# Optimization experiments

Hardware: AMD Instinct MI355X
Metric: run time of the kernel (lower is better)

The kernel has to match this reference:

```python
import jax, jax.numpy as jnp
import numpy as np

H, D, HID, DIN = 2, 32, 64, 128
NQ, NA, NK = 100000, 200000, 200000
E_KQ, E_QK, E_QA, E_AQ = 800000, 800000, 400000, 400000
EP, EN = 100000, 100000


def setup_inputs() -> dict:
    key = jax.random.key(0)
    ks = jax.random.split(key, 32)
    f = lambda i, shape, s=0.05: jax.random.normal(ks[i], shape, dtype=jnp.float32) * s
    ri = lambda i, n, hi: jax.random.randint(ks[i], (n,), 0, hi)
    return {
        'xq': f(0, (NQ, DIN), 1.0), 'xa': f(1, (NA, DIN), 1.0), 'xk': f(2, (NK, DIN), 1.0),
        'lin_w': f(3, (3, DIN, HID)), 'lin_b': f(4, (3, HID)),
        'k_w': f(5, (3, HID, HID)), 'k_b': f(6, (3, HID)),
        'q_w': f(7, (3, HID, HID)), 'q_b': f(8, (3, HID)),
        'v_w': f(9, (3, HID, HID)), 'v_b': f(10, (3, HID)),
        'a_w': f(11, (3, HID, HID)), 'a_b': f(12, (3, HID)),
        'a_rel': f(13, (4, H, D, D), 0.2), 'm_rel': f(14, (4, H, D, D), 0.2),
        'p_rel': jnp.ones((4, H), dtype=jnp.float32),  # PyG init: ones
        'skip': jnp.ones((3,), dtype=jnp.float32),     # PyG init: ones
        'ei_kq_src': ri(15, E_KQ, NK), 'ei_kq_dst': ri(16, E_KQ, NQ),
        'ei_qk_src': ri(17, E_QK, NQ), 'ei_qk_dst': ri(18, E_QK, NA * 0 + NK),
        'ei_qa_src': ri(19, E_QA, NQ), 'ei_qa_dst': ri(20, E_QA, NA),
        'ei_aq_src': ri(21, E_AQ, NA), 'ei_aq_dst': ri(22, E_AQ, NQ),
        'pos_src': ri(23, EP, NQ), 'pos_dst': ri(24, EP, NA),
        'neg_src': ri(25, EN, NQ), 'neg_dst': ri(26, EN, NA),
    }


def _seg_softmax(alpha, dst, n):
    # softmax over incoming edges per destination node (per head)
    m = jax.ops.segment_max(alpha, dst, num_segments=n)
    m = jnp.where(jnp.isfinite(m), m, 0.0)
    e = jnp.exp(alpha - m[dst])
    s = jax.ops.segment_sum(e, dst, num_segments=n)
    return e / (s[dst] + 1e-16)


def hgt_forward(xq, xa, xk, lin_w, lin_b, k_w, k_b, q_w, q_b, v_w, v_b, a_w, a_b,
                a_rel, m_rel, p_rel, skip, edges):
    # node types: 0=question, 1=answer, 2=knowledge
    xs = [jax.nn.relu(x @ lin_w[i] + lin_b[i]) for i, x in enumerate([xq, xa, xk])]
    ns = [x.shape[0] for x in xs]
    k = [(x @ k_w[i] + k_b[i]).reshape(-1, H, D) for i, x in enumerate(xs)]
    q = [(x @ q_w[i] + q_b[i]).reshape(-1, H, D) for i, x in enumerate(xs)]
    v = [(x @ v_w[i] + v_b[i]).reshape(-1, H, D) for i, x in enumerate(xs)]
    out = [jnp.zeros((n, H, D), dtype=xs[0].dtype) for n in ns]
    scale = 1.0 / jnp.sqrt(jnp.float32(D))
    for st, dt, r, es, ed in edges:
        # per-edge-type head-wise key/value transforms (applied at node level)
        k_rel = jnp.einsum('nhd,hde->nhe', k[st], a_rel[r])
        v_rel = jnp.einsum('nhd,hde->nhe', v[st], m_rel[r])
        alpha = (q[dt][ed] * k_rel[es]).sum(-1) * p_rel[r] * scale  # [E,H]
        a = _seg_softmax(alpha, ed, ns[dt])
        msg = a[:, :, None] * v_rel[es]  # [E,H,D]
        out[dt] = out[dt] + jax.ops.segment_sum(msg, ed, num_segments=ns[dt])
    z = []
    for i in range(3):
        o = jax.nn.gelu(out[i].reshape(-1, H * D), approximate=False) @ a_w[i] + a_b[i]
        beta = jax.nn.sigmoid(skip[i])
        z.append(beta * o + (1.0 - beta) * xs[i])
    return z  # [z_question, z_answer, z_knowledge]; note: HGT.forward never applies self.lin


def reference(xq, xa, xk, lin_w, lin_b, k_w, k_b, q_w, q_b, v_w, v_b, a_w, a_b,
              a_rel, m_rel, p_rel, skip,
              ei_kq_src, ei_kq_dst, ei_qk_src, ei_qk_dst, ei_qa_src, ei_qa_dst,
              ei_aq_src, ei_aq_dst, pos_src, pos_dst, neg_src, neg_dst):
    edges = [
        (2, 0, 0, ei_kq_src, ei_kq_dst),  # knowledge -> question
        (0, 2, 1, ei_qk_src, ei_qk_dst),  # question -> knowledge
        (0, 1, 2, ei_qa_src, ei_qa_dst),  # question -> answer
        (1, 0, 3, ei_aq_src, ei_aq_dst),  # answer -> question
    ]
    zq, za, zk = hgt_forward(xq, xa, xk, lin_w, lin_b, k_w, k_b, q_w, q_b, v_w, v_b,
                             a_w, a_b, a_rel, m_rel, p_rel, skip, edges)
    pos_pred = jax.nn.sigmoid((zq[pos_src] * za[pos_dst]).sum(-1))
    neg_pred = jax.nn.sigmoid((zq[neg_src] * za[neg_dst]).sum(-1))
    return (pos_pred, neg_pred, zq, za, zk)
```

## Files before the change

### kernel.cpp

```cpp
#include <hip/hip_runtime.h>
#include <math.h>

namespace {

constexpr int NQn = 100000, NAn = 200000, NKn = 200000;
constexpr int EPc = 100000, ENc = 100000;
constexpr int ETOT = 2400000, NSEG = 600000;
constexpr int LIN_THREADS = 7813 * 256;

constexpr long XSB_OFF  = 0;
constexpr long OUTB_OFF = 16000000;
constexpr long QBF_OFF  = 32000000;
constexpr long KV_OFF   = 48000000;
constexpr long ZB_OFF   = 86500000;
constexpr long WTB_OFF  = 96200000;
constexpr long WFB_OFF  = 96250000;
constexpr long INT_OFF  = 96300000;
constexpr long DEG_I  = 0;
constexpr long OFFS_I = 600064;
constexpr long PART_I = 1200128;
constexpr long RANK_I = 1201152;
constexpr long CSRC_I = 3601152;

constexpr int LINT_U = 0;
constexpr int QT_U   = 24576;
constexpr int AT_U   = 36864;
constexpr int WFT_U  = 49152;

__constant__ long c_rbase[4] = {0, 200000, 300032, 400064};

typedef __attribute__((ext_vector_type(8))) short bf16x8;
typedef __attribute__((ext_vector_type(4))) float f32x4;
typedef __attribute__((ext_vector_type(4))) unsigned int u32x4;
typedef __attribute__((ext_vector_type(2))) unsigned int u32x2;

__device__ inline f32x4 mfma16(bf16x8 a, bf16x8 b, f32x4 c) {
    return __builtin_amdgcn_mfma_f32_16x16x32_bf16(a, b, c, 0, 0, 0);
}

__device__ inline float gelu_f(float x) {
    return 0.5f * x * (1.0f + erff(x * 0.7071067811865475f));
}
__device__ inline float bf2f(unsigned short u) {
    return __uint_as_float(((unsigned)u) << 16);
}
__device__ inline unsigned short f2bf(float f) {
    unsigned u = __float_as_uint(f);
    return (unsigned short)((u + 0x7fffu + ((u >> 16) & 1u)) >> 16);
}

__device__ inline void type_of_block128(int b, int& t, int& n0) {
    if (b < 782)       { t = 0; n0 = b * 128; }
    else if (b < 2345) { t = 1; n0 = (b - 782) * 128; }
    else               { t = 2; n0 = (b - 2345) * 128; }
}
__device__ inline void type_of_block64(int b, int& t, int& n0) {
    if (b < 1563)      { t = 0; n0 = b * 64; }
    else if (b < 4688) { t = 1; n0 = (b - 1563) * 64; }
    else               { t = 2; n0 = (b - 4688) * 64; }
}

template<int K>
__device__ inline void stage_bf16(unsigned short* lds, const unsigned short* src,
                                  int n0, int n, int tid)
{
    constexpr int CPR = K / 8;
    for (int c = tid; c < 128 * CPR; c += 256) {
        int row = c / CPR, kc = c % CPR;
        int node = n0 + row; if (node > n - 1) node = n - 1;
        uint4 v = *(const uint4*)&src[(long)node * K + kc * 8];
        int byte = (row * K + kc * 8) * 2;
        *(uint4*)((char*)lds + (byte ^ ((row & 7) << 4))) = v;
    }
}

__device__ inline void stage_out_gelu(unsigned short* lds, const unsigned short* src,
                                      int n0, int n, int tid)
{
    for (int c = tid; c < 128 * 8; c += 256) {
        int row = c >> 3, kc = c & 7;
        int node = n0 + row; if (node > n - 1) node = n - 1;
        uint4 v = *(const uint4*)&src[(long)node * 64 + kc * 8];
        float f0 = gelu_f(bf2f((unsigned short)(v.x & 0xffffu)));
        float f1 = gelu_f(bf2f((unsigned short)(v.x >> 16)));
        float f2 = gelu_f(bf2f((unsigned short)(v.y & 0xffffu)));
        float f3 = gelu_f(bf2f((unsigned short)(v.y >> 16)));
        float f4 = gelu_f(bf2f((unsigned short)(v.z & 0xffffu)));
        float f5 = gelu_f(bf2f((unsigned short)(v.z >> 16)));
        float f6 = gelu_f(bf2f((unsigned short)(v.w & 0xffffu)));
        float f7 = gelu_f(bf2f((unsigned short)(v.w >> 16)));
        uint4 o;
        o.x = (unsigned)f2bf(f0) | ((unsigned)f2bf(f1) << 16);
        o.y = (unsigned)f2bf(f2) | ((unsigned)f2bf(f3) << 16);
        o.z = (unsigned)f2bf(f4) | ((unsigned)f2bf(f5) << 16);
        o.w = (unsigned)f2bf(f6) | ((unsigned)f2bf(f7) << 16);
        int byte = (row * 64 + kc * 8) * 2;
        *(uint4*)((char*)lds + (byte ^ ((row & 7) << 4))) = o;
    }
}

template<int K, int ROWS>
__device__ inline void stage_f32_nt(unsigned short* lds, const float* src,
                                    int n0, int n, int tid)
{
    constexpr int CPR = K / 8;
    for (int c = tid; c < ROWS * CPR; c += 256) {
        int row = c / CPR, kc = c % CPR;
        int node = n0 + row; if (node > n - 1) node = n - 1;
        const f32x4* sp = (const f32x4*)&src[(long)node * K + kc * 8];
        f32x4 f0 = __builtin_nontemporal_load(sp);
        f32x4 f1 = __builtin_nontemporal_load(sp + 1);
        uint4 v;
        v.x = (unsigned)f2bf(f0.x) | ((unsigned)f2bf(f0.y) << 16);
        v.y = (unsigned)f2bf(f0.z) | ((unsigned)f2bf(f0.w) << 16);
        v.z = (unsigned)f2bf(f1.x) | ((unsigned)f2bf(f1.y) << 16);
        v.w = (unsigned)f2bf(f1.z) | ((unsigned)f2bf(f1.w) << 16);
        int byte = (row * K + kc * 8) * 2;
        *(uint4*)((char*)lds + (byte ^ ((row & 7) << 4))) = v;
    }
}

template<int N, int K>
__device__ inline void stage_w(unsigned short* lds, const unsigned short* wt, int tid)
{
    constexpr int CPR = K / 8;
    for (int c = tid; c < N * CPR; c += 256) {
        int nr = c / CPR, kc = c % CPR;
        uint4 v = *(const uint4*)&wt[nr * K + kc * 8];
        int byte = (nr * K + kc * 8) * 2;
        *(uint4*)((char*)lds + (byte ^ ((nr & 7) << 4))) = v;
    }
}

template<int K, int NF, int MF>
__device__ inline void mfma_coreT(const unsigned short* ldsX, const unsigned short* ldsW,
                                  f32x4 (&acc)[MF][NF], int lane, int w)
{
    const int lrow = lane & 15, lk = (lane >> 4) * 8;
    #pragma unroll
    for (int ks = 0; ks < K / 32; ++ks) {
        bf16x8 a[MF], b[NF];
        #pragma unroll
        for (int mf = 0; mf < MF; ++mf) {
            int row = w * (16 * MF) + mf * 16 + lrow;
            int byte = (row * K + ks * 32 + lk) * 2;
            a[mf] = *(const bf16x8*)((const char*)ldsX + (byte ^ ((row & 7) << 4)));
        }
        #pragma unroll
        for (int nf = 0; nf < NF; ++nf) {
            int nr = nf * 16 + lrow;
            int byte = (nr * K + ks * 32 + lk) * 2;
            b[nf] = *(const bf16x8*)((const char*)ldsW + (byte ^ ((nr & 7) << 4)));
        }
        #pragma unroll
        for (int mf = 0; mf < MF; ++mf)
            #pragma unroll
            for (int nf = 0; nf < NF; ++nf)
                acc[mf][nf] = mfma16(b[nf], a[mf], acc[mf][nf]);
    }
}

__device__ inline void edge_map(int gid,
                                const int* __restrict__ s0, const int* __restrict__ d0,
                                const int* __restrict__ s1, const int* __restrict__ d1,
                                const int* __restrict__ s2, const int* __restrict__ d2,
                                const int* __restrict__ s3, const int* __restrict__ d3,
                                int& seg, int& s)
{
    if (gid < 800000)       { seg = d0[gid];                    s = s0[gid]; }
    else if (gid < 1600000) { seg = 100000 + d1[gid - 800000];  s = s1[gid - 800000]; }
    else if (gid < 2000000) { seg = 300000 + d2[gid - 1600000]; s = s2[gid - 1600000]; }
    else                    { seg = 500000 + d3[gid - 2000000]; s = s3[gid - 2000000]; }
}
__device__ inline int edge_seg(int gid,
                               const int* __restrict__ d0, const int* __restrict__ d1,
                               const int* __restrict__ d2, const int* __restrict__ d3)
{
    if (gid < 800000)       return d0[gid];
    else if (gid < 1600000) return 100000 + d1[gid - 800000];
    else if (gid < 2000000) return 300000 + d2[gid - 1600000];
    else                    return 500000 + d3[gid - 2000000];
}

__global__ void prep_count(const float* __restrict__ lin_w, const float* __restrict__ q_w,
                           const float* __restrict__ a_w,
                           const float* __restrict__ kw, const float* __restrict__ kb,
                           const float* __restrict__ vw, const float* __restrict__ vb,
                           const float* __restrict__ a_rel, const float* __restrict__ m_rel,
                           unsigned short* __restrict__ wtb, float* __restrict__ wfb,
                           const int* __restrict__ d0, const int* __restrict__ d1,
                           const int* __restrict__ d2, const int* __restrict__ d3,
                           int* __restrict__ deg, int* __restrict__ rank)
{
    const int tid = threadIdx.x;
    if (blockIdx.x < 4) {
        const int r = blockIdx.x;
        const int st_tab[4] = {2, 0, 0, 1};
        const int st = st_tab[r];
        for (int idx = tid; idx < 8192; idx += 256) {
            int d = idx >> 7, c = idx & 127;
            int i = c >> 1, which = c & 1;
            int h = i >> 5, e = i & 31;
            const float* w   = (which ? vw : kw) + st * 4096;
            const float* rel = (which ? m_rel : a_rel) + r * 2048;
            float s = 0.f;
            #pragma unroll
            for (int c32 = 0; c32 < 32; ++c32)
                s += w[d * 64 + h * 32 + c32] * rel[h * 1024 + c32 * 32 + e];
            wtb[WFT_U + r * 8192 + c * 64 + d] = f2bf(s);
        }
        for (int idx = tid; idx < 128; idx += 256) {
            int i = idx >> 1, which = idx & 1;
            int h = i >> 5, e = i & 31;
            const float* b   = (which ? vb : kb) + st * 64;
            const float* rel = (which ? m_rel : a_rel) + r * 2048;
            float s = 0.f;
            #pragma unroll
            for (int c32 = 0; c32 < 32; ++c32)
                s += b[h * 32 + c32] * rel[h * 1024 + c32 * 32 + e];
            wfb[r * 128 + idx] = s;
        }
    } else if (blockIdx.x < 196) {
        int i = (blockIdx.x - 4) * 256 + tid;
        if (i < 24576) {
            int t = i / 8192, rem = i % 8192, nn = rem >> 7, kk = rem & 127;
            wtb[LINT_U + i] = f2bf(lin_w[t * 8192 + kk * 64 + nn]);
        } else if (i < 36864) {
            int j = i - 24576;
            int t = j / 4096, rem = j % 4096, nn = rem >> 6, kk = rem & 63;
            wtb[QT_U + j] = f2bf(q_w[t * 4096 + kk * 64 + nn]);
        } else if (i < 49152) {
            int j = i - 36864;
            int t = j / 4096, rem = j % 4096, nn = rem >> 6, kk = rem & 63;
            wtb[AT_U + j] = f2bf(a_w[t * 4096 + kk * 64 + nn]);
        }
    } else {
        int gid = (blockIdx.x - 196) * 256 + tid;
        if (gid < ETOT) {
            int seg = edge_seg(gid, d0, d1, d2, d3);
            rank[gid] = atomicAdd(&deg[seg], 1);
        }
    }
}

__global__ void __launch_bounds__(256)
lin_fill(const int* __restrict__ s0, const int* __restrict__ d0,
         const int* __restrict__ s1, const int* __restrict__ d1,
         const int* __restrict__ s2, const int* __restrict__ d2,
         const int* __restrict__ s3, const int* __restrict__ d3,
         const int* __restrict__ off, const int* __restrict__ rank,
         int* __restrict__ csrc,
         const float* __restrict__ xq, const float* __restrict__ xa,
         const float* __restrict__ xk, const unsigned short* __restrict__ wtb,
         const float* __restrict__ lin_b, unsigned short* __restrict__ xsb)
{
    __shared__ unsigned short ldsX[64 * 128];
    __shared__ unsigned short ldsW[64 * 128];
    const int tid = threadIdx.x;
    const int gid = blockIdx.x * 256 + tid;

    int segA, sA;
    edge_map(gid, s0, d0, s1, d1, s2, d2, s3, d3, segA, sA);
    int rkA = rank[gid];
    int offA = off[segA];
    const int gidB = gid + LIN_THREADS;
    const bool hasB = gidB < ETOT;
    int segB = 0, sB = 0, rkB = 0, offB = 0;
    if (hasB) {
        edge_map(gidB, s0, d0, s1, d1, s2, d2, s3, d3, segB, sB);
        rkB = rank[gidB];
        offB = off[segB];
    }

    int t, n0; type_of_block64(blockIdx.x, t, n0);
    const int cnt[3] = {NQn, NAn, NKn};
    const long noff[3] = {0, NQn, NQn + NAn};
    const float* X = (t == 0) ? xq : (t == 1) ? xa : xk;
    const int n = cnt[t];

    stage_w<64, 128>(ldsW, wtb + LINT_U + t * 8192, tid);
    stage_f32_nt<128, 64>(ldsX, X, n0, n, tid);
    __syncthreads();

    csrc[offA + rkA] = sA;
    if (hasB) csrc[offB + rkB] = sB;

    const int w = tid >> 6, lane = tid & 63;
    f32x4 acc[1][4] = {};
    mfma_coreT<128, 4, 1>(ldsX, ldsW, acc, lane, w);

    const int nodeL = lane & 15, colG = (lane >> 4) * 4;
    int node = n0 + w * 16 + nodeL;
    if (node < n) {
        #pragma unroll
        for (int nf = 0; nf < 4; ++nf) {
            int col0 = nf * 16 + colG;
            float4 bv = *(const float4*)&lin_b[t * 64 + col0];
            ushort4 o;
            o.x = f2bf(fmaxf(acc[0][nf][0] + bv.x, 0.f));
            o.y = f2bf(fmaxf(acc[0][nf][1] + bv.y, 0.f));
            o.z = f2bf(fmaxf(acc[0][nf][2] + bv.z, 0.f));
            o.w = f2bf(fmaxf(acc[0][nf][3] + bv.w, 0.f));
            *(ushort4*)&xsb[(noff[t] + node) * 64 + col0] = o;
        }
    }
}

__global__ void __launch_bounds__(256)
qkv_split(const unsigned short* __restrict__ xsb, const unsigned short* __restrict__ wtb,
          const float* __restrict__ q_b, const float* __restrict__ wfb,
          unsigned short* __restrict__ qbf, unsigned short* __restrict__ kvb)
{
    __shared__ unsigned short ldsX[128 * 64];
    __shared__ unsigned short ldsW[128 * 64];
    const int cnt[3] = {NQn, NAn, NKn};
    const long noff[3] = {0, NQn, NQn + NAn};
    const int tid = threadIdx.x;
    const int w = tid >> 6, lane = tid & 63;
    const int nodeL = lane & 15, colG = (lane >> 4) * 4;
    const int b = blockIdx.x;

    if (b < 3908) {
        int t, n0; type_of_block128(b, t, n0);
        const int n = cnt[t];
        stage_bf16<64>(ldsX, xsb + noff[t] * 64, n0, n, tid);
        stage_w<64, 64>(ldsW, wtb + QT_U + t * 4096, tid);
        __syncthreads();

        f32x4 acc[2][4] = {};
        mfma_coreT<64, 4, 2>(ldsX, ldsW, acc, lane, w);
        #pragma unroll
        for (int mf = 0; mf < 2; ++mf) {
            int node = n0 + w * 32 + mf * 16 + nodeL;
            if (node < n) {
                #pragma unroll
                for (int nf = 0; nf < 4; ++nf) {
                    int col0 = nf * 16 + colG;
                    float4 bv = *(const float4*)&q_b[t * 64 + col0];
                    ushort4 o;
                    o.x = f2bf(acc[mf][nf][0] + bv.x);
                    o.y = f2bf(acc[mf][nf][1] + bv.y);
                    o.z = f2bf(acc[mf][nf][2] + bv.z);
                    o.w = f2bf(acc[mf][nf][3] + bv.w);
                    *(ushort4*)&qbf[(noff[t] + node) * 64 + col0] = o;
                }
            }
        }
    } else {
        int kb = b - 3908, r, lb;
        if (kb < 1563)      { r = 0; lb = kb; }
        else if (kb < 2345) { r = 1; lb = kb - 1563; }
        else if (kb < 3127) { r = 2; lb = kb - 2345; }
        else                { r = 3; lb = kb - 3127; }
        const int stt[4] = {2, 0, 0, 1};
        const int st = stt[r];
        const int n0 = lb * 128;
        const int n = cnt[st];
        const long rb = c_rbase[r];

        stage_bf16<64>(ldsX, xsb + noff[st] * 64, n0, n, tid);
        stage_w<128, 64>(ldsW, wtb + WFT_U + r * 8192, tid);
        __syncthreads();

        f32x4 acc[2][8] = {};
        mfma_coreT<64, 8, 2>(ldsX, ldsW, acc, lane, w);
        #pragma unroll
        for (int mf = 0; mf < 2; ++mf) {
            int node = n0 + w * 32 + mf * 16 + nodeL;
            if (node < n) {
                #pragma unroll
                for (int nf = 0; nf < 8; ++nf) {
                    int col0 = nf * 16 + colG;
                    float4 bv = *(const float4*)&wfb[r * 128 + col0];
                    ushort4 o;
                    o.x = f2bf(acc[mf][nf][0] + bv.x);
                    o.y = f2bf(acc[mf][nf][1] + bv.y);
                    o.z = f2bf(acc[mf][nf][2] + bv.z);
                    o.w = f2bf(acc[mf][nf][3] + bv.w);
                    *(ushort4*)&kvb[(rb + node) * 128 + col0] = o;
                }
            }
        }
    }
}

__global__ void __launch_bounds__(256)
head_mfma(const unsigned short* __restrict__ outb, const unsigned short* __restrict__ xsb,
          const unsigned short* __restrict__ wtb, const float* __restrict__ a_b,
          const float* __restrict__ skip, float* __restrict__ z,
          unsigned short* __restrict__ zb)
{
    __shared__ unsigned short ldsX[128 * 64];
    __shared__ unsigned short ldsW[64 * 64];
    int t, n0; type_of_block128(blockIdx.x, t, n0);
    const int cnt[3] = {NQn, NAn, NKn};
    const long noff[3] = {0, NQn, NQn + NAn};
    const long zoff[3] = {200000L, 6600000L, 19400000L};
    const int n = cnt[t];
    const int tid = threadIdx.x;

    stage_w<64, 64>(ldsW, wtb + AT_U + t * 4096, tid);
    stage_out_gelu(ldsX, outb + noff[t] * 64, n0, n, tid);
    __syncthreads();

    const int w = tid >> 6, lane = tid & 63;
    f32x4 acc[2][4] = {};
    mfma_coreT<64, 4, 2>(ldsX, ldsW, acc, lane, w);

    const float beta = 1.f / (1.f + expf(-skip[t]));
    const int nodeL = lane & 15, colG = (lane >> 4) * 4;
    #pragma unroll
    for (int mf = 0; mf < 2; ++mf) {
        int node = n0 + w * 32 + mf * 16 + nodeL;
        if (node < n) {
            #pragma unroll
            for (int nf = 0; nf < 4; ++nf) {
                int col0 = nf * 16 + colG;
                float4 bv = *(const float4*)&a_b[t * 64 + col0];
                ushort4 rv = *(const ushort4*)&xsb[(noff[t] + node) * 64 + col0];
                f32x4 o;
                o.x = beta * (acc[mf][nf][0] + bv.x) + (1.f - beta) * bf2f(rv.x);
                o.y = beta * (acc[mf][nf][1] + bv.y) + (1.f - beta) * bf2f(rv.y);
                o.z = beta * (acc[mf][nf][2] + bv.z) + (1.f - beta) * bf2f(rv.z);
                o.w = beta * (acc[mf][nf][3] + bv.w) + (1.f - beta) * bf2f(rv.w);
                __builtin_nontemporal_store(o, (f32x4*)&z[zoff[t] + (long)node * 64 + col0]);
                if (t < 2) {
                    ushort4 p;
                    p.x = f2bf(o.x); p.y = f2bf(o.y); p.z = f2bf(o.z); p.w = f2bf(o.w);
                    long zrow = (t == 0) ? (long)node : 100000L + node;
                    *(ushort4*)&zb[zrow * 64 + col0] = p;
                }
            }
        }
    }
}

__global__ void scan1(const int* __restrict__ in, int* __restrict__ out,
                      int* __restrict__ part, int n)
{
    __shared__ int lds[256];
    const int tid = threadIdx.x;
    const int base = blockIdx.x * 1024 + tid * 4;
    int v[4];
    #pragma unroll
    for (int k = 0; k < 4; ++k) v[k] = (base + k < n) ? in[base + k] : 0;
    int tsum = v[0] + v[1] + v[2] + v[3];
    lds[tid] = tsum;
    __syncthreads();
    for (int off = 1; off < 256; off <<= 1) {
        int t = (tid >= off) ? lds[tid - off] : 0;
        __syncthreads();
        lds[tid] += t;
        __syncthreads();
    }
    int excl = lds[tid] - tsum;
    #pragma unroll
    for (int k = 0; k < 4; ++k) {
        if (base + k < n) out[base + k] = excl;
        excl += v[k];
    }
    if (tid == 255) part[blockIdx.x] = lds[255];
}

__global__ void scan2(int* __restrict__ part, int nb)
{
    __shared__ int lds[256];
    const int tid = threadIdx.x;
    const int base = tid * 4;
    int v[4];
    #pragma unroll
    for (int k = 0; k < 4; ++k) v[k] = (base + k < nb) ? part[base + k] : 0;
    int tsum = v[0] + v[1] + v[2] + v[3];
    lds[tid] = tsum;
    __syncthreads();
    for (int off = 1; off < 256; off <<= 1) {
        int t = (tid >= off) ? lds[tid - off] : 0;
        __syncthreads();
        lds[tid] += t;
        __syncthreads();
    }
    int excl = lds[tid] - tsum;
    #pragma unroll
    for (int k = 0; k < 4; ++k) {
        if (base + k < nb) part[base + k] = excl;
        excl += v[k];
    }
}

__global__ void scan3(int* __restrict__ off, const int* __restrict__ part, int n, int E)
{
    int i = blockIdx.x * 256 + threadIdx.x;
    if (i < n) off[i] += part[i >> 10];
    if (i == 0) off[n] = E;
}

__device__ inline void attn_node(const int* __restrict__ csrc, int begin, int end,
                                 const unsigned short* __restrict__ kvt,
                                 const float qv[4], int j, float res[4])
{
    float ss = 0.f, a0 = 0.f, a1 = 0.f, a2 = 0.f, a3 = 0.f;

    for (int t = begin; t < end; t += 4) {
        bool v1 = (t + 1 < end), v2 = (t + 2 < end), v3 = (t + 3 < end);
        int s0 = csrc[t];
        int s1 = csrc[v1 ? t + 1 : t];
        int s2 = csrc[v2 ? t + 2 : t];
        int s3 = csrc[v3 ? t + 3 : t];
        uint4 k0 = *(const uint4*)(kvt + (long)s0 * 128 + j * 8);
        uint4 k1 = *(const uint4*)(kvt + (long)s1 * 128 + j * 8);
        uint4 k2 = *(const uint4*)(kvt + (long)s2 * 128 + j * 8);
        uint4 k3 = *(const uint4*)(kvt + (long)s3 * 128 + j * 8);

        float p0 = __uint_as_float(k0.x << 16) * qv[0] + __uint_as_float(k0.y << 16) * qv[1]
                 + __uint_as_float(k0.z << 16) * qv[2] + __uint_as_float(k0.w << 16) * qv[3];
        float p1 = __uint_as_float(k1.x << 16) * qv[0] + __uint_as_float(k1.y << 16) * qv[1]
                 + __uint_as_float(k1.z << 16) * qv[2] + __uint_as_float(k1.w << 16) * qv[3];
        float p2 = __uint_as_float(k2.x << 16) * qv[0] + __uint_as_float(k2.y << 16) * qv[1]
                 + __uint_as_float(k2.z << 16) * qv[2] + __uint_as_float(k2.w << 16) * qv[3];
        float p3 = __uint_as_float(k3.x << 16) * qv[0] + __uint_as_float(k3.y << 16) * qv[1]
                 + __uint_as_float(k3.z << 16) * qv[2] + __uint_as_float(k3.w << 16) * qv[3];

        p0 += __shfl_xor(p0, 1);  p1 += __shfl_xor(p1, 1);
        p2 += __shfl_xor(p2, 1);  p3 += __shfl_xor(p3, 1);
        p0 += __shfl_xor(p0, 2);  p1 += __shfl_xor(p1, 2);
        p2 += __shfl_xor(p2, 2);  p3 += __shfl_xor(p3, 2);
        p0 += __shfl_xor(p0, 4);  p1 += __shfl_xor(p1, 4);
        p2 += __shfl_xor(p2, 4);  p3 += __shfl_xor(p3, 4);

        float w0 = exp2f(fminf(p0, 115.f));
        float w1 = v1 ? exp2f(fminf(p1, 115.f)) : 0.f;
        float w2 = v2 ? exp2f(fminf(p2, 115.f)) : 0.f;
        float w3 = v3 ? exp2f(fminf(p3, 115.f)) : 0.f;

        ss += (w0 + w1) + (w2 + w3);
        a0 += w0 * __uint_as_float(k0.x & 0xffff0000u) + w1 * __uint_as_float(k1.x & 0xffff0000u)
            + w2 * __uint_as_float(k2.x & 0xffff0000u) + w3 * __uint_as_float(k3.x & 0xffff0000u);
        a1 += w0 * __uint_as_float(k0.y & 0xffff0000u) + w1 * __uint_as_float(k1.y & 0xffff0000u)
            + w2 * __uint_as_float(k2.y & 0xffff0000u) + w3 * __uint_as_float(k3.y & 0xffff0000u);
        a2 += w0 * __uint_as_float(k0.z & 0xffff0000u) + w1 * __uint_as_float(k1.z & 0xffff0000u)
            + w2 * __uint_as_float(k2.z & 0xffff0000u) + w3 * __uint_as_float(k3.z & 0xffff0000u);
        a3 += w0 * __uint_as_float(k0.w & 0xffff0000u) + w1 * __uint_as_float(k1.w & 0xffff0000u)
            + w2 * __uint_as_float(k2.w & 0xffff0000u) + w3 * __uint_as_float(k3.w & 0xffff0000u);
    }

    float inv = 1.f / (ss + 1e-16f);
    res[0] = a0 * inv; res[1] = a1 * inv; res[2] = a2 * inv; res[3] = a3 * inv;
}

__global__ void __launch_bounds__(256)
attn_all(const int* __restrict__ off, const int* __restrict__ csrc,
         const unsigned short* __restrict__ qbf, const unsigned short* __restrict__ kv,
         const float* __restrict__ prel, float scale, unsigned short* __restrict__ outb)
{
    const int tid = threadIdx.x;
    const int nid = blockIdx.x * 16 + (tid >> 4);
    const int j = tid & 15;
    const int h = j >> 3;
    const float l2e = 1.4426950408889634f;

    long row; int segA, segB = -1; long kbA, kbB = 0; float psA, psB = 0.f;
    if (nid < 100000) {
        row = nid;
        segA = nid;            kbA = c_rbase[0]; psA = prel[0 + h] * scale * l2e;
        segB = 500000 + nid;   kbB = c_rbase[3]; psB = prel[6 + h] * scale * l2e;
    } else if (nid < 300000) {
        int kk = nid - 100000;
        row = 300000 + kk;
        segA = 100000 + kk;    kbA = c_rbase[1]; psA = prel[2 + h] * scale * l2e;
    } else {
        int aa = nid - 300000;
        row = 100000 + aa;
        segA = 300000 + aa;    kbA = c_rbase[2]; psA = prel[4 + h] * scale * l2e;
    }

    u32x2 qw = __builtin_nontemporal_load((const u32x2*)&qbf[row * 64 + 4 * j]);
    float qraw[4] = {bf2f((unsigned short)(qw.x & 0xffffu)),
                     bf2f((unsigned short)(qw.x >> 16)),
                     bf2f((unsigned short)(qw.y & 0xffffu)),
                     bf2f((unsigned short)(qw.y >> 16))};

    float res[4];
    {
        float qv[4] = {qraw[0] * psA, qraw[1] * psA, qraw[2] * psA, qraw[3] * psA};
        attn_node(csrc, off[segA], off[segA + 1], kv + kbA * 128, qv, j, res);
    }
    if (segB >= 0) {
        float qv[4] = {qraw[0] * psB, qraw[1] * psB, qraw[2] * psB, qraw[3] * psB};
        float r2[4];
        attn_node(csrc, off[segB], off[segB + 1], kv + kbB * 128, qv, j, r2);
        res[0] += r2[0]; res[1] += r2[1]; res[2] += r2[2]; res[3] += r2[3];
    }

    u32x2 o;
    o.x = (unsigned)f2bf(res[0]) | ((unsigned)f2bf(res[1]) << 16);
    o.y = (unsigned)f2bf(res[2]) | ((unsigned)f2bf(res[3]) << 16);
    __builtin_nontemporal_store(o, (u32x2*)&outb[row * 64 + 4 * j]);
}

__global__ void pred_all(const int* __restrict__ psrc, const int* __restrict__ pdst,
                         const int* __restrict__ nsrc, const int* __restrict__ ndst,
                         const unsigned short* __restrict__ zb, float* __restrict__ out)
{
    int t = blockIdx.x * 256 + threadIdx.x;
    int g = t >> 3, lane = t & 7;
    if (g >= EPc + ENc) return;
    int s, d;
    if (g < EPc) { s = psrc[g]; d = pdst[g]; }
    else         { int gg = g - EPc; s = nsrc[gg]; d = ndst[gg]; }
    uint4 zs = *(const uint4*)&zb[(long)s * 64 + lane * 8];
    uint4 zd = *(const uint4*)&zb[(100000L + d) * 64 + lane * 8];
    float p = 0.f;
    p += bf2f((unsigned short)(zs.x & 0xffffu)) * bf2f((unsigned short)(zd.x & 0xffffu));
    p += bf2f((unsigned short)(zs.x >> 16))     * bf2f((unsigned short)(zd.x >> 16));
    p += bf2f((unsigned short)(zs.y & 0xffffu)) * bf2f((unsigned short)(zd.y & 0xffffu));
    p += bf2f((unsigned short)(zs.y >> 16))     * bf2f((unsigned short)(zd.y >> 16));
    p += bf2f((unsigned short)(zs.z & 0xffffu)) * bf2f((unsigned short)(zd.z & 0xffffu));
    p += bf2f((unsigned short)(zs.z >> 16))     * bf2f((unsigned short)(zd.z >> 16));
    p += bf2f((unsigned short)(zs.w & 0xffffu)) * bf2f((unsigned short)(zd.w & 0xffffu));
    p += bf2f((unsigned short)(zs.w >> 16))     * bf2f((unsigned short)(zd.w >> 16));
    p += __shfl_xor(p, 1);
    p += __shfl_xor(p, 2);
    p += __shfl_xor(p, 4);
    if (lane == 0) out[g] = 1.f / (1.f + expf(-p));
}

}

extern "C" void kernel_launch(void* const* d_in, const int* in_sizes, int n_in,
                              void* d_out, int out_size, void* d_ws, size_t ws_size,
                              hipStream_t stream)
{
    const float* xq    = (const float*)d_in[0];
    const float* xa    = (const float*)d_in[1];
    const float* xk    = (const float*)d_in[2];
    const float* lin_w = (const float*)d_in[3];
    const float* lin_b = (const float*)d_in[4];
    const float* k_w   = (const float*)d_in[5];
    const float* k_b   = (const float*)d_in[6];
    const float* q_w   = (const float*)d_in[7];
    const float* q_b   = (const float*)d_in[8];
    const float* v_w   = (const float*)d_in[9];
    const float* v_b   = (const float*)d_in[10];
    const float* a_w   = (const float*)d_in[11];
    const float* a_b   = (const float*)d_in[12];
    const float* a_rel = (const float*)d_in[13];
    const float* m_rel = (const float*)d_in[14];
    const float* p_rel = (const float*)d_in[15];
    const float* skip  = (const float*)d_in[16];
    const int* esrc[4] = {(const int*)d_in[17], (const int*)d_in[19], (const int*)d_in[21], (const int*)d_in[23]};
    const int* edst[4] = {(const int*)d_in[18], (const int*)d_in[20], (const int*)d_in[22], (const int*)d_in[24]};
    const int* pos_src = (const int*)d_in[25];
    const int* pos_dst = (const int*)d_in[26];
    const int* neg_src = (const int*)d_in[27];
    const int* neg_dst = (const int*)d_in[28];

    float* ws   = (float*)d_ws;
    float* outp = (float*)d_out;
    int*   wi   = (int*)(ws + INT_OFF);
    unsigned short* xsb  = (unsigned short*)(ws + XSB_OFF);
    unsigned short* outb = (unsigned short*)(ws + OUTB_OFF);
    unsigned short* qbf  = (unsigned short*)(ws + QBF_OFF);
    unsigned short* kvb  = (unsigned short*)(ws + KV_OFF);
    unsigned short* zbb  = (unsigned short*)(ws + ZB_OFF);
    unsigned short* wtb  = (unsigned short*)(ws + WTB_OFF);
    float*          wfb  = ws + WFB_OFF;

    hipMemsetAsync(wi + DEG_I, 0, 600000L * sizeof(int), stream);

    prep_count<<<196 + 9375, 256, 0, stream>>>(
        lin_w, q_w, a_w, k_w, k_b, v_w, v_b, a_rel, m_rel, wtb, wfb,
        edst[0], edst[1], edst[2], edst[3], wi + DEG_I, wi + RANK_I);

    const int nb = (NSEG + 1023) / 1024;
    scan1<<<nb, 256, 0, stream>>>(wi + DEG_I, wi + OFFS_I, wi + PART_I, NSEG);
    scan2<<<1, 256, 0, stream>>>(wi + PART_I, nb);
    scan3<<<(NSEG + 255) / 256, 256, 0, stream>>>(wi + OFFS_I, wi + PART_I, NSEG, ETOT);

    lin_fill<<<7813, 256, 0, stream>>>(
        esrc[0], edst[0], esrc[1], edst[1], esrc[2], edst[2], esrc[3], edst[3],
        wi + OFFS_I, wi + RANK_I, wi + CSRC_I,
        xq, xa, xk, wtb, lin_b, xsb);

    qkv_split<<<8598, 256, 0, stream>>>(xsb, wtb, q_b, wfb, qbf, kvb);

    const float scale = 0.17677669529663687f;
    attn_all<<<31250, 256, 0, stream>>>(wi + OFFS_I, wi + CSRC_I, qbf, kvb,
                                        p_rel, scale, outb);

    head_mfma<<<3908, 256, 0, stream>>>(outb, xsb, wtb, a_b, skip, outp, zbb);

    pred_all<<<(200000 * 8 + 255) / 256, 256, 0, stream>>>(
        pos_src, pos_dst, neg_src, neg_dst, zbb, outp);
}
```

Baseline: 531.9 us.

## Fuse input linear into degree-count kernel and move CSR fill into QKV kernel

Moves the input projection (lin) into the first kernel, interleaving its blocks with the edge degree-counting blocks. Each lin block now transposes and converts lin_w from fp32 in LDS itself instead of reading a pre-converted bf16 copy. The CSR source fill moves from the lin kernel into the QKV projection kernel, which removes one kernel launch and overlaps atomic counting with MFMA work. In exchange, every lin block repeats the weight transpose with scattered 2-byte LDS stores, and the QKV blocks take on the extra scattered index writes.

```diff
diff --git a/kernel.cpp b/kernel.cpp
--- a/kernel.cpp
+++ b/kernel.cpp
@@ -6,7 +6,7 @@
 constexpr int NQn = 100000, NAn = 200000, NKn = 200000;
 constexpr int EPc = 100000, ENc = 100000;
 constexpr int ETOT = 2400000, NSEG = 600000;
-constexpr int LIN_THREADS = 7813 * 256;
+constexpr int QKV_THREADS = 8598 * 256;
 
 constexpr long XSB_OFF  = 0;
 constexpr long OUTB_OFF = 16000000;
@@ -22,16 +22,14 @@
 constexpr long RANK_I = 1201152;
 constexpr long CSRC_I = 3601152;
 
-constexpr int LINT_U = 0;
-constexpr int QT_U   = 24576;
-constexpr int AT_U   = 36864;
-constexpr int WFT_U  = 49152;
+constexpr int QT_U   = 0;
+constexpr int AT_U   = 12288;
+constexpr int WFT_U  = 24576;
 
 __constant__ long c_rbase[4] = {0, 200000, 300032, 400064};
 
 typedef __attribute__((ext_vector_type(8))) short bf16x8;
 typedef __attribute__((ext_vector_type(4))) float f32x4;
-typedef __attribute__((ext_vector_type(4))) unsigned int u32x4;
 typedef __attribute__((ext_vector_type(2))) unsigned int u32x2;
 
 __device__ inline f32x4 mfma16(bf16x8 a, bf16x8 b, f32x4 c) {
@@ -132,6 +130,21 @@
     }
 }
 
+__device__ inline void stage_wT_f32(unsigned short* lds, const float* w, int tid)
+{
+    for (int c = tid * 4; c < 8192; c += 1024) {
+        int kk = c >> 6, nn0 = c & 63;
+        float4 v = *(const float4*)&w[kk * 64 + nn0];
+        float vals[4] = {v.x, v.y, v.z, v.w};
+        #pragma unroll
+        for (int i = 0; i < 4; ++i) {
+            int nn = nn0 + i;
+            int byte = (nn * 128 + kk) * 2;
+            *(unsigned short*)((char*)lds + (byte ^ ((nn & 7) << 4))) = f2bf(vals[i]);
+        }
+    }
+}
+
 template<int K, int NF, int MF>
 __device__ inline void mfma_coreT(const unsigned short* ldsX, const unsigned short* ldsW,
                                   f32x4 (&acc)[MF][NF], int lane, int w)
@@ -182,19 +195,32 @@
     else                    return 500000 + d3[gid - 2000000];
 }
 
-__global__ void prep_count(const float* __restrict__ lin_w, const float* __restrict__ q_w,
-                           const float* __restrict__ a_w,
-                           const float* __restrict__ kw, const float* __restrict__ kb,
-                           const float* __restrict__ vw, const float* __restrict__ vb,
-                           const float* __restrict__ a_rel, const float* __restrict__ m_rel,
-                           unsigned short* __restrict__ wtb, float* __restrict__ wfb,
-                           const int* __restrict__ d0, const int* __restrict__ d1,
-                           const int* __restrict__ d2, const int* __restrict__ d3,
-                           int* __restrict__ deg, int* __restrict__ rank)
-{
+__global__ void __launch_bounds__(256)
+lin_prep_count(const float* __restrict__ xq, const float* __restrict__ xa,
+               const float* __restrict__ xk, const float* __restrict__ lin_w,
+               const float* __restrict__ lin_b, unsigned short* __restrict__ xsb,
+               const float* __restrict__ q_w, const float* __restrict__ a_w,
+               const float* __restrict__ kw, const float* __restrict__ kb,
+               const float* __restrict__ vw, const float* __restrict__ vb,
+               const float* __restrict__ a_rel, const float* __restrict__ m_rel,
+               unsigned short* __restrict__ wtb, float* __restrict__ wfb,
+               const int* __restrict__ d0, const int* __restrict__ d1,
+               const int* __restrict__ d2, const int* __restrict__ d3,
+               int* __restrict__ deg, int* __restrict__ rank)
+{
+    __shared__ unsigned short ldsX[64 * 128];
+    __shared__ unsigned short ldsW[64 * 128];
+    const int b = blockIdx.x;
     const int tid = threadIdx.x;
-    if (blockIdx.x < 4) {
-        const int r = blockIdx.x;
+
+    int linb = -1, cntb = -1;
+    if (b < 15626) {
+        if (b & 1) cntb = b >> 1;
+        else       linb = b >> 1;
+    } else if (b < 17188) {
+        cntb = 7813 + (b - 15626);
+    } else if (b < 17192) {
+        const int r = b - 17188;
         const int st_tab[4] = {2, 0, 0, 1};
         const int st = st_tab[r];
         for (int idx = tid; idx < 8192; idx += 256) {
@@ -212,78 +238,46 @@
         for (int idx = tid; idx < 128; idx += 256) {
             int i = idx >> 1, which = idx & 1;
             int h = i >> 5, e = i & 31;
-            const float* b   = (which ? vb : kb) + st * 64;
+            const float* bb  = (which ? vb : kb) + st * 64;
             const float* rel = (which ? m_rel : a_rel) + r * 2048;
             float s = 0.f;
             #pragma unroll
             for (int c32 = 0; c32 < 32; ++c32)
-                s += b[h * 32 + c32] * rel[h * 1024 + c32 * 32 + e];
+                s += bb[h * 32 + c32] * rel[h * 1024 + c32 * 32 + e];
             wfb[r * 128 + idx] = s;
         }
-    } else if (blockIdx.x < 196) {
-        int i = (blockIdx.x - 4) * 256 + tid;
-        if (i < 24576) {
-            int t = i / 8192, rem = i % 8192, nn = rem >> 7, kk = rem & 127;
-            wtb[LINT_U + i] = f2bf(lin_w[t * 8192 + kk * 64 + nn]);
-        } else if (i < 36864) {
-            int j = i - 24576;
-            int t = j / 4096, rem = j % 4096, nn = rem >> 6, kk = rem & 63;
-            wtb[QT_U + j] = f2bf(q_w[t * 4096 + kk * 64 + nn]);
-        } else if (i < 49152) {
-            int j = i - 36864;
+        return;
+    } else {
+        int i = (b - 17192) * 256 + tid;
+        if (i < 12288) {
+            int t = i / 4096, rem = i % 4096, nn = rem >> 6, kk = rem & 63;
+            wtb[QT_U + i] = f2bf(q_w[t * 4096 + kk * 64 + nn]);
+        } else {
+            int j = i - 12288;
             int t = j / 4096, rem = j % 4096, nn = rem >> 6, kk = rem & 63;
             wtb[AT_U + j] = f2bf(a_w[t * 4096 + kk * 64 + nn]);
         }
-    } else {
-        int gid = (blockIdx.x - 196) * 256 + tid;
+        return;
+    }
+
+    if (cntb >= 0) {
+        int gid = cntb * 256 + tid;
         if (gid < ETOT) {
             int seg = edge_seg(gid, d0, d1, d2, d3);
             rank[gid] = atomicAdd(&deg[seg], 1);
         }
-    }
-}
-
-__global__ void __launch_bounds__(256)
-lin_fill(const int* __restrict__ s0, const int* __restrict__ d0,
-         const int* __restrict__ s1, const int* __restrict__ d1,
-         const int* __restrict__ s2, const int* __restrict__ d2,
-         const int* __restrict__ s3, const int* __restrict__ d3,
-         const int* __restrict__ off, const int* __restrict__ rank,
-         int* __restrict__ csrc,
-         const float* __restrict__ xq, const float* __restrict__ xa,
-         const float* __restrict__ xk, const unsigned short* __restrict__ wtb,
-         const float* __restrict__ lin_b, unsigned short* __restrict__ xsb)
-{
-    __shared__ unsigned short ldsX[64 * 128];
-    __shared__ unsigned short ldsW[64 * 128];
-    const int tid = threadIdx.x;
-    const int gid = blockIdx.x * 256 + tid;
-
-    int segA, sA;
-    edge_map(gid, s0, d0, s1, d1, s2, d2, s3, d3, segA, sA);
-    int rkA = rank[gid];
-    int offA = off[segA];
-    const int gidB = gid + LIN_THREADS;
-    const bool hasB = gidB < ETOT;
-    int segB = 0, sB = 0, rkB = 0, offB = 0;
-    if (hasB) {
-        edge_map(gidB, s0, d0, s1, d1, s2, d2, s3, d3, segB, sB);
-        rkB = rank[gidB];
-        offB = off[segB];
-    }
-
-    int t, n0; type_of_block64(blockIdx.x, t, n0);
+        return;
+    }
+
+    int t, n0; type_of_block64(linb, t, n0);
     const int cnt[3] = {NQn, NAn, NKn};
     const long noff[3] = {0, NQn, NQn + NAn};
     const float* X = (t == 0) ? xq : (t == 1) ? xa : xk;
     const int n = cnt[t];
 
-    stage_w<64, 128>(ldsW, wtb + LINT_U + t * 8192, tid);
+    stage_wT_f32(ldsW, lin_w + (long)t * 8192, tid);
     stage_f32_nt<128, 64>(ldsX, X, n0, n, tid);
     __syncthreads();
-
-    csrc[offA + rkA] = sA;
-    if (hasB) csrc[offB + rkB] = sB;
 
     const int w = tid >> 6, lane = tid & 63;
     f32x4 acc[1][4] = {};
@@ -307,18 +301,38 @@
 }
 
 __global__ void __launch_bounds__(256)
-qkv_split(const unsigned short* __restrict__ xsb, const unsigned short* __restrict__ wtb,
-          const float* __restrict__ q_b, const float* __restrict__ wfb,
-          unsigned short* __restrict__ qbf, unsigned short* __restrict__ kvb)
+qkv_fill(const int* __restrict__ s0, const int* __restrict__ d0,
+         const int* __restrict__ s1, const int* __restrict__ d1,
+         const int* __restrict__ s2, const int* __restrict__ d2,
+         const int* __restrict__ s3, const int* __restrict__ d3,
+         const int* __restrict__ off, const int* __restrict__ rank,
+         int* __restrict__ csrc,
+         const unsigned short* __restrict__ xsb, const unsigned short* __restrict__ wtb,
+         const float* __restrict__ q_b, const float* __restrict__ wfb,
+         unsigned short* __restrict__ qbf, unsigned short* __restrict__ kvb)
 {
     __shared__ unsigned short ldsX[128 * 64];
     __shared__ unsigned short ldsW[128 * 64];
     const int cnt[3] = {NQn, NAn, NKn};
     const long noff[3] = {0, NQn, NQn + NAn};
     const int tid = threadIdx.x;
+    const int gid = blockIdx.x * 256 + tid;
     const int w = tid >> 6, lane = tid & 63;
     const int nodeL = lane & 15, colG = (lane >> 4) * 4;
     const int b = blockIdx.x;
+
+    int segA, sA;
+    edge_map(gid, s0, d0, s1, d1, s2, d2, s3, d3, segA, sA);
+    int rkA = rank[gid];
+    int offA = off[segA];
+    const int gidB = gid + QKV_THREADS;
+    const bool hasB = gidB < ETOT;
+    int segB = 0, sB = 0, rkB = 0, offB = 0;
+    if (hasB) {
+        edge_map(gidB, s0, d0, s1, d1, s2, d2, s3, d3, segB, sB);
+        rkB = rank[gidB];
+        offB = off[segB];
+    }
 
     if (b < 3908) {
         int t, n0; type_of_block128(b, t, n0);
@@ -326,6 +340,9 @@
         stage_bf16<64>(ldsX, xsb + noff[t] * 64, n0, n, tid);
         stage_w<64, 64>(ldsW, wtb + QT_U + t * 4096, tid);
         __syncthreads();
+
+        csrc[offA + rkA] = sA;
+        if (hasB) csrc[offB + rkB] = sB;
 
         f32x4 acc[2][4] = {};
         mfma_coreT<64, 4, 2>(ldsX, ldsW, acc, lane, w);
@@ -361,6 +378,9 @@
         stage_bf16<64>(ldsX, xsb + noff[st] * 64, n0, n, tid);
         stage_w<128, 64>(ldsW, wtb + WFT_U + r * 8192, tid);
         __syncthreads();
+
+        csrc[offA + rkA] = sA;
+        if (hasB) csrc[offB + rkB] = sB;
 
         f32x4 acc[2][8] = {};
         mfma_coreT<64, 8, 2>(ldsX, ldsW, acc, lane, w);
@@ -667,8 +687,9 @@
 
     hipMemsetAsync(wi + DEG_I, 0, 600000L * sizeof(int), stream);
 
-    prep_count<<<196 + 9375, 256, 0, stream>>>(
-        lin_w, q_w, a_w, k_w, k_b, v_w, v_b, a_rel, m_rel, wtb, wfb,
+    lin_prep_count<<<17288, 256, 0, stream>>>(
+        xq, xa, xk, lin_w, lin_b, xsb,
+        q_w, a_w, k_w, k_b, v_w, v_b, a_rel, m_rel, wtb, wfb,
         edst[0], edst[1], edst[2], edst[3], wi + DEG_I, wi + RANK_I);
 
     const int nb = (NSEG + 1023) / 1024;
@@ -676,12 +697,10 @@
     scan2<<<1, 256, 0, stream>>>(wi + PART_I, nb);
     scan3<<<(NSEG + 255) / 256, 256, 0, stream>>>(wi + OFFS_I, wi + PART_I, NSEG, ETOT);
 
-    lin_fill<<<7813, 256, 0, stream>>>(
+    qkv_fill<<<8598, 256, 0, stream>>>(
         esrc[0], edst[0], esrc[1], edst[1], esrc[2], edst[2], esrc[3], edst[3],
         wi + OFFS_I, wi + RANK_I, wi + CSRC_I,
-        xq, xa, xk, wtb, lin_b, xsb);
-
-    qkv_split<<<8598, 256, 0, stream>>>(xsb, wtb, q_b, wfb, qbf, kvb);
+        xsb, wtb, q_b, wfb, qbf, kvb);
 
     const float scale = 0.17677669529663687f;
     attn_all<<<31250, 256, 0, stream>>>(wi + OFFS_I, wi + CSRC_I, qbf, kvb,
```

New measurement: 579.2 us. +8.9%, slower.
